# Performance work log

Hardware: AMD Instinct MI355X
Metric: run time of the kernel (lower is better)

The kernel has to match this reference:

```python
import jax, jax.numpy as jnp
import numpy as np

B, N, DIM, H, DH = 4, 16384, 256, 8, 32
INNER = H * DH
SCALE = DH ** -0.5


def setup_inputs() -> dict:
    key = jax.random.key(0)
    ks = jax.random.split(key, 15)
    g = lambda k, shape, s=0.02: jax.random.normal(k, shape, dtype=jnp.float32) * s
    return {
        "states": jax.random.normal(ks[0], (B, N, DIM), dtype=jnp.float32),
        "agent_qs": jax.random.normal(ks[1], (B, N, DIM), dtype=jnp.float32),
        "obs": jax.random.normal(ks[2], (B, N, DIM), dtype=jnp.float32),
        "Wq": g(ks[3], (DIM, INNER)), "bq": g(ks[4], (INNER,)),
        "Wk": g(ks[5], (DIM, INNER)), "bk": g(ks[6], (INNER,)),
        "Wv": g(ks[7], (DIM, INNER)), "bv": g(ks[8], (INNER,)),
        "wq_attn": g(ks[9], (DH,), 0.1),
        "wk_attn": g(ks[10], (DH,), 0.1),
        "Wr": g(ks[11], (DH, DH)), "br": g(ks[12], (DH,)),
        "Wout": g(ks[13], (INNER, DIM)), "bout": g(ks[14], (DIM,)),
    }


def _heads(t):
    # [b, n, h*d] -> [b, h, n, d]
    b, n, _ = t.shape
    return t.reshape(b, n, H, DH).transpose(0, 2, 1, 3)


def reference(states, agent_qs, obs, Wq, bq, Wk, bk, Wv, bv,
              wq_attn, wk_attn, Wr, br, Wout, bout):
    q = _heads(jnp.abs(states @ Wq + bq))   # b h n d
    k = _heads(agent_qs @ Wk + bk)          # b h n d
    v = _heads(obs @ Wv + bv)               # b h n d

    # additive attention pooling for global query
    q_attn = jax.nn.softmax(jnp.einsum('bhnd,d->bhn', q, wq_attn) * SCALE, axis=-1)
    global_q = jnp.einsum('bhn,bhnd->bhd', q_attn, q)  # b h d

    # gate keys with global query, pool against ORIGINAL k (k_aggr)
    k_gated = k * global_q[:, :, None, :]
    k_attn = jax.nn.softmax(jnp.einsum('bhnd,d->bhn', k_gated, wk_attn) * SCALE, axis=-1)
    global_k = jnp.einsum('bhn,bhnd->bhd', k_attn, k)  # b h d

    u = v * global_k[:, :, None, :]
    r = u @ Wr + br + q                      # b h n d
    r = r.transpose(0, 2, 1, 3).reshape(r.shape[0], r.shape[2], INNER)  # b n (h d)
    return r @ Wout + bout
```

## Files before the change

### kernel.cpp

```cpp
#include <hip/hip_runtime.h>
#include <hip/hip_bf16.h>

#define B_   4
#define N_   16384
#define T_   65536
static constexpr float SCALE_F = 0.17677669529663687f;

typedef __attribute__((ext_vector_type(8))) short bf16x8;
typedef __attribute__((ext_vector_type(4))) float f32x4;

static __device__ __forceinline__ unsigned pk2bf(float lo, float hi) {
    __hip_bfloat162 t = __float22bfloat162_rn(make_float2(lo, hi));
    union { __hip_bfloat162 h; unsigned u; } c; c.h = t; return c.u;
}
static __device__ __forceinline__ unsigned short f2bf(float f) {
    unsigned u = __float_as_uint(f);
    u += 0x7fffu + ((u >> 16) & 1u);
    return (unsigned short)(u >> 16);
}
static __device__ __forceinline__ void gl_lds16(const void* g, void* l) {
    __builtin_amdgcn_global_load_lds(
        (const __attribute__((address_space(1))) unsigned int*)g,
        (__attribute__((address_space(3))) unsigned int*)l, 16, 0, 0);
}

__global__ __launch_bounds__(256) void prep_w(
    const float* __restrict__ Wq, const float* __restrict__ Wk,
    const float* __restrict__ Wv, unsigned short* __restrict__ Wt)
{
    const int m = blockIdx.x;
    const float* W = (m == 0) ? Wq : (m == 1) ? Wk : Wv;
    unsigned short* dst = Wt + (size_t)m * 65536 + (size_t)threadIdx.x * 256;
    #pragma unroll 4
    for (int kb = 0; kb < 32; ++kb) {
        float v[8];
        #pragma unroll
        for (int e = 0; e < 8; ++e) v[e] = W[(kb*8 + e)*256 + threadIdx.x];
        uint4 w;
        w.x = pk2bf(v[0], v[1]); w.y = pk2bf(v[2], v[3]);
        w.z = pk2bf(v[4], v[5]); w.w = pk2bf(v[6], v[7]);
        *reinterpret_cast<uint4*>(dst + kb*8) = w;
    }
}

__global__ __launch_bounds__(256) void proj_mfma(
    const float* __restrict__ states, const float* __restrict__ agent_qs,
    const float* __restrict__ obs, const unsigned short* __restrict__ Wt,
    const float* __restrict__ bq, const float* __restrict__ bk,
    const float* __restrict__ bv,
    unsigned short* __restrict__ q_bf, unsigned short* __restrict__ k_bf,
    unsigned short* __restrict__ v_bf)
{
    __shared__ __align__(16) float As[2][64*32];

    const int tid = threadIdx.x;
    const int z  = blockIdx.y;
    const int t0 = blockIdx.x * 64;

    const float* X = (z == 0) ? states : (z == 1) ? agent_qs : obs;
    const unsigned short* Bt = Wt + (size_t)z * 65536;
    const float* bias = (z == 0) ? bq : (z == 1) ? bk : bv;
    unsigned short* Y = (z == 0) ? q_bf : (z == 1) ? k_bf : v_bf;
    const bool doabs = (z == 0);

    const int wid = tid >> 6, lane = tid & 63;
    const int l15 = lane & 15, g = lane >> 4;
    const int wc = wid;

    int ntrue[4];
    #pragma unroll
    for (int ni = 0; ni < 4; ++ni) {
        int np = ni*16 + l15;
        int c = (np & 32) | ((np & 12) << 1) | ((np & 16) >> 2) | (np & 3);
        ntrue[ni] = wc*64 + c;
    }

    const int srow_lane = lane >> 3;
    const int schunk = (lane & 7) ^ (lane >> 3);
    auto stageA = [&](int buf, int k0) {
        #pragma unroll
        for (int i = 0; i < 2; ++i) {
            int r = (wid*2 + i)*8 + srow_lane;
            const float* src = X + (size_t)(t0 + r)*256 + k0 + schunk*4;
            gl_lds16(src, &As[buf][(wid*2 + i)*256]);
        }
    };
    auto loadB = [&](bf16x8* breg, int k0) {
        #pragma unroll
        for (int ni = 0; ni < 4; ++ni)
            breg[ni] = *reinterpret_cast<const bf16x8*>(
                Bt + (size_t)ntrue[ni]*256 + k0 + g*8);
    };
    auto readA = [&](int buf, bf16x8* areg) {
        #pragma unroll
        for (int mi = 0; mi < 4; ++mi) {
            int m = mi*16 + l15;
            int x = m & 7;
            f32x4 lo = *reinterpret_cast<const f32x4*>(&As[buf][m*32 + ((2*g)  ^x)*4]);
            f32x4 hi = *reinterpret_cast<const f32x4*>(&As[buf][m*32 + ((2*g+1)^x)*4]);
            union { unsigned u[4]; bf16x8 v; } cc;
            cc.u[0] = pk2bf(lo[0], lo[1]);
            cc.u[1] = pk2bf(lo[2], lo[3]);
            cc.u[2] = pk2bf(hi[0], hi[1]);
            cc.u[3] = pk2bf(hi[2], hi[3]);
            areg[mi] = cc.v;
        }
    };

    f32x4 acc[4][4];
    #pragma unroll
    for (int mi = 0; mi < 4; ++mi)
        #pragma unroll
        for (int ni = 0; ni < 4; ++ni) acc[mi][ni] = (f32x4){0.f,0.f,0.f,0.f};

    bf16x8 bcur[4], bnxt[4];
    stageA(0, 0);
    loadB(bcur, 0);
    __syncthreads();

    int cur = 0;
    for (int s = 0; s < 8; ++s) {
        if (s < 7) { stageA(cur ^ 1, (s+1)*32); loadB(bnxt, (s+1)*32); }
        bf16x8 a[4];
        readA(cur, a);
        #pragma unroll
        for (int mi = 0; mi < 4; ++mi)
            #pragma unroll
            for (int ni = 0; ni < 4; ++ni)
                acc[mi][ni] = __builtin_amdgcn_mfma_f32_16x16x32_bf16(
                    bcur[ni], a[mi], acc[mi][ni], 0, 0, 0);
        __syncthreads();
        #pragma unroll
        for (int ni = 0; ni < 4; ++ni) bcur[ni] = bnxt[ni];
        cur ^= 1;
    }

    #pragma unroll
    for (int mi = 0; mi < 4; ++mi) {
        int m = t0 + mi*16 + l15;
        #pragma unroll
        for (int s = 0; s < 2; ++s) {
            int colb = wc*64 + s*32 + g*8;
            float4 b0 = *reinterpret_cast<const float4*>(bias + colb);
            float4 b1 = *reinterpret_cast<const float4*>(bias + colb + 4);
            float y0 = acc[mi][2*s  ][0] + b0.x;
            float y1 = acc[mi][2*s  ][1] + b0.y;
            float y2 = acc[mi][2*s  ][2] + b0.z;
            float y3 = acc[mi][2*s  ][3] + b0.w;
            float y4 = acc[mi][2*s+1][0] + b1.x;
            float y5 = acc[mi][2*s+1][1] + b1.y;
            float y6 = acc[mi][2*s+1][2] + b1.z;
            float y7 = acc[mi][2*s+1][3] + b1.w;
            if (doabs) {
                y0 = fabsf(y0); y1 = fabsf(y1); y2 = fabsf(y2); y3 = fabsf(y3);
                y4 = fabsf(y4); y5 = fabsf(y5); y6 = fabsf(y6); y7 = fabsf(y7);
            }
            uint4 pk;
            pk.x = pk2bf(y0, y1); pk.y = pk2bf(y2, y3);
            pk.z = pk2bf(y4, y5); pk.w = pk2bf(y6, y7);
            *reinterpret_cast<uint4*>(Y + (size_t)m*256 + colb) = pk;
        }
    }
}

__global__ __launch_bounds__(512) void pool_partial(
    const unsigned short* __restrict__ data,
    const float* __restrict__ wqa, const float* __restrict__ wka,
    const float* __restrict__ gq_in, float* __restrict__ part, int mode)
{
    const int bh = blockIdx.x, ch = blockIdx.y;
    const int b = bh >> 3, h = bh & 7;
    const int tid = threadIdx.x;

    __shared__ float coef[32];
    __shared__ float s_red[8];
    __shared__ float a_red[8][32];

    if (tid < 32) {
        float cc = (mode == 0) ? wqa[tid] : gq_in[bh*32 + tid] * wka[tid];
        coef[tid] = cc * SCALE_F;
    }
    __syncthreads();
    float cf[32];
    #pragma unroll
    for (int d = 0; d < 32; ++d) cf[d] = coef[d];

    float s = 0.f;
    float acc[32];
    #pragma unroll
    for (int d = 0; d < 32; ++d) acc[d] = 0.f;

    const unsigned short* base = data + (size_t)b * N_ * 256 + h * 32;
    for (int n = ch*2048 + tid; n < (ch + 1)*2048; n += 512) {
        const uint4* p = reinterpret_cast<const uint4*>(base + (size_t)n * 256);
        float qv[32];
        #pragma unroll
        for (int gg = 0; gg < 4; ++gg) {
            uint4 r = p[gg];
            unsigned w0 = r.x, w1 = r.y, w2 = r.z, w3 = r.w;
            qv[gg*8+0] = __uint_as_float(w0 << 16);
            qv[gg*8+1] = __uint_as_float(w0 & 0xffff0000u);
            qv[gg*8+2] = __uint_as_float(w1 << 16);
            qv[gg*8+3] = __uint_as_float(w1 & 0xffff0000u);
            qv[gg*8+4] = __uint_as_float(w2 << 16);
            qv[gg*8+5] = __uint_as_float(w2 & 0xffff0000u);
            qv[gg*8+6] = __uint_as_float(w3 << 16);
            qv[gg*8+7] = __uint_as_float(w3 & 0xffff0000u);
        }
        float l = 0.f;
        #pragma unroll
        for (int d = 0; d < 32; ++d) l = fmaf(qv[d], cf[d], l);
        float e = expf(l);
        s += e;
        #pragma unroll
        for (int d = 0; d < 32; ++d) acc[d] = fmaf(e, qv[d], acc[d]);
    }

    #pragma unroll
    for (int off = 1; off < 64; off <<= 1) {
        s += __shfl_xor(s, off);
        #pragma unroll
        for (int d = 0; d < 32; ++d) acc[d] += __shfl_xor(acc[d], off);
    }
    const int wave = tid >> 6, lane = tid & 63;
    if (lane == 0) {
        s_red[wave] = s;
        #pragma unroll
        for (int d = 0; d < 32; ++d) a_red[wave][d] = acc[d];
    }
    __syncthreads();
    if (tid < 32) {
        float num = 0.f, den = 0.f;
        #pragma unroll
        for (int w2 = 0; w2 < 8; ++w2) { num += a_red[w2][tid]; den += s_red[w2]; }
        part[(size_t)(bh*8 + ch)*40 + tid] = num;
        if (tid == 0) part[(size_t)(bh*8 + ch)*40 + 32] = den;
    }
}

__global__ __launch_bounds__(64) void pool_final(
    const float* __restrict__ part, float* __restrict__ outv)
{
    const int bh = blockIdx.x, d = threadIdx.x;
    if (d >= 32) return;
    float num = 0.f, den = 0.f;
    #pragma unroll
    for (int c = 0; c < 8; ++c) {
        num += part[(size_t)(bh*8 + c)*40 + d];
        den += part[(size_t)(bh*8 + c)*40 + 32];
    }
    outv[bh*32 + d] = num / den;
}

__global__ __launch_bounds__(256) void build_s1(
    const float* __restrict__ Wr, const float* __restrict__ br,
    const float* __restrict__ Wout, const float* __restrict__ bout,
    float* __restrict__ S1t, float* __restrict__ cvec)
{
    const int i = blockIdx.x, j = threadIdx.x;
    if (i < 256) {
        const int h = i >> 5, dd = i & 31;
        float s = 0.f;
        #pragma unroll 8
        for (int dp = 0; dp < 32; ++dp)
            s = fmaf(Wr[dd*32 + dp], Wout[(h*32 + dp)*256 + j], s);
        S1t[(size_t)j*256 + i] = s;
    } else {
        float cj = bout[j];
        for (int r = 0; r < 256; ++r) cj = fmaf(br[r & 31], Wout[r*256 + j], cj);
        cvec[j] = cj;
    }
}

__global__ __launch_bounds__(256) void build_wcat_t(
    const float* __restrict__ gk, const float* __restrict__ S1t,
    const float* __restrict__ Wout, unsigned short* __restrict__ Wcat_t)
{
    const int b = blockIdx.x, n = blockIdx.y, k = threadIdx.x;
    unsigned short* dst = Wcat_t + (size_t)(b*256 + n) * 512;
    dst[k]       = f2bf(gk[b*256 + k] * S1t[(size_t)n*256 + k]);
    dst[k + 256] = f2bf(Wout[(size_t)k*256 + n]);
}

__global__ __launch_bounds__(256) void out_mfma(
    const unsigned short* __restrict__ v_bf, const unsigned short* __restrict__ q_bf,
    const unsigned short* __restrict__ Wcat_t, const float* __restrict__ cvec,
    float* __restrict__ out)
{
    __shared__ __align__(16) unsigned short As[2][64*32];

    const int tid = threadIdx.x;
    const int t0 = blockIdx.x * 64;
    const int b  = t0 >> 14;
    const unsigned short* Wb = Wcat_t + (size_t)b * 256 * 512;

    const int wid = tid >> 6, lane = tid & 63;
    const int l15 = lane & 15, g = lane >> 4, wc = wid;

    const int sr = wid*16 + (lane >> 2);
    const int stc = (lane & 3) ^ (sr & 3) ^ ((sr >> 2) & 3);
    auto stageA = [&](int buf, int k0) {
        const unsigned short* src = (k0 < 256) ? v_bf : q_bf;
        int ks = k0 & 255;
        gl_lds16(src + (size_t)(t0 + sr)*256 + ks + stc*8, &As[buf][wid*512]);
    };
    auto loadB = [&](bf16x8* breg, int k0) {
        #pragma unroll
        for (int ni = 0; ni < 4; ++ni) {
            int nt = wc*64 + ni*16 + l15;
            breg[ni] = *reinterpret_cast<const bf16x8*>(
                Wb + (size_t)nt*512 + k0 + g*8);
        }
    };
    auto readA = [&](int buf, bf16x8* areg) {
        #pragma unroll
        for (int mi = 0; mi < 4; ++mi) {
            int m = mi*16 + l15;
            int cc = g ^ (m & 3) ^ ((m >> 2) & 3);
            areg[mi] = *reinterpret_cast<const bf16x8*>(&As[buf][m*32 + cc*8]);
        }
    };

    f32x4 acc[4][4];
    #pragma unroll
    for (int mi = 0; mi < 4; ++mi)
        #pragma unroll
        for (int ni = 0; ni < 4; ++ni) acc[mi][ni] = (f32x4){0.f,0.f,0.f,0.f};

    bf16x8 bcur[4], bnxt[4];
    stageA(0, 0);
    loadB(bcur, 0);
    __syncthreads();

    int cur = 0;
    for (int s = 0; s < 16; ++s) {
        if (s < 15) { stageA(cur ^ 1, (s+1)*32); loadB(bnxt, (s+1)*32); }
        bf16x8 a[4];
        readA(cur, a);
        #pragma unroll
        for (int mi = 0; mi < 4; ++mi)
            #pragma unroll
            for (int ni = 0; ni < 4; ++ni)
                acc[mi][ni] = __builtin_amdgcn_mfma_f32_16x16x32_bf16(
                    bcur[ni], a[mi], acc[mi][ni], 0, 0, 0);
        __syncthreads();
        #pragma unroll
        for (int ni = 0; ni < 4; ++ni) bcur[ni] = bnxt[ni];
        cur ^= 1;
    }

    #pragma unroll
    for (int ni = 0; ni < 4; ++ni) {
        int colb = wc*64 + ni*16 + g*4;
        float4 cv = *reinterpret_cast<const float4*>(cvec + colb);
        #pragma unroll
        for (int mi = 0; mi < 4; ++mi) {
            int m = t0 + mi*16 + l15;
            float4 o;
            o.x = acc[mi][ni][0] + cv.x;
            o.y = acc[mi][ni][1] + cv.y;
            o.z = acc[mi][ni][2] + cv.z;
            o.w = acc[mi][ni][3] + cv.w;
            *reinterpret_cast<float4*>(out + (size_t)m*256 + colb) = o;
        }
    }
}

extern "C" void kernel_launch(void* const* d_in, const int* in_sizes, int n_in,
                              void* d_out, int out_size, void* d_ws, size_t ws_size,
                              hipStream_t stream)
{
    const float* states   = (const float*)d_in[0];
    const float* agent_qs = (const float*)d_in[1];
    const float* obs      = (const float*)d_in[2];
    const float* Wq   = (const float*)d_in[3];
    const float* bq   = (const float*)d_in[4];
    const float* Wk   = (const float*)d_in[5];
    const float* bk   = (const float*)d_in[6];
    const float* Wv   = (const float*)d_in[7];
    const float* bv   = (const float*)d_in[8];
    const float* wq_attn = (const float*)d_in[9];
    const float* wk_attn = (const float*)d_in[10];
    const float* Wr   = (const float*)d_in[11];
    const float* br   = (const float*)d_in[12];
    const float* Wout = (const float*)d_in[13];
    const float* bout = (const float*)d_in[14];
    float* out = (float*)d_out;

    char* w = (char*)d_ws;
    unsigned short* q_bf = (unsigned short*)w; w += (size_t)T_ * 256 * 2;
    unsigned short* k_bf = (unsigned short*)w; w += (size_t)T_ * 256 * 2;
    unsigned short* v_bf = (unsigned short*)w; w += (size_t)T_ * 256 * 2;
    unsigned short* Wt_bf   = (unsigned short*)w; w += (size_t)3 * 65536 * 2;
    unsigned short* Wcat_t  = (unsigned short*)w; w += (size_t)4 * 256 * 512 * 2;
    float* gq   = (float*)w; w += 1024 * sizeof(float);
    float* gk   = (float*)w; w += 1024 * sizeof(float);
    float* part = (float*)w; w += (size_t)256 * 40 * sizeof(float);
    float* S1t  = (float*)w; w += (size_t)256 * 256 * sizeof(float);
    float* cvec = (float*)w; w += 256 * sizeof(float);

    prep_w<<<dim3(3), 256, 0, stream>>>(Wq, Wk, Wv, Wt_bf);
    proj_mfma<<<dim3(1024, 3), 256, 0, stream>>>(
        states, agent_qs, obs, Wt_bf, bq, bk, bv, q_bf, k_bf, v_bf);
    pool_partial<<<dim3(32, 8), 512, 0, stream>>>(q_bf, wq_attn, wk_attn, gq, part, 0);
    pool_final<<<dim3(32), 64, 0, stream>>>(part, gq);
    pool_partial<<<dim3(32, 8), 512, 0, stream>>>(k_bf, wq_attn, wk_attn, gq, part, 1);
    pool_final<<<dim3(32), 64, 0, stream>>>(part, gk);
    build_s1<<<dim3(257), 256, 0, stream>>>(Wr, br, Wout, bout, S1t, cvec);
    build_wcat_t<<<dim3(4, 256), 256, 0, stream>>>(gk, S1t, Wout, Wcat_t);
    out_mfma<<<dim3(1024), 256, 0, stream>>>(v_bf, q_bf, Wcat_t, cvec, out);
}
```

Before: 219.0 us.

## Triple-buffer GEMM staging and fold small reduction kernels into neighbors

Both MFMA GEMM kernels move from double to triple-buffered LDS staging. They use explicit vmcnt waits and raw barriers, so async global-to-LDS loads run two steps ahead and the full __syncthreads drain is gone. The pool_final kernels are removed, with their reductions folded into the next pool_partial and build_wcat_t. build_s1 is merged into the weight-prep kernel, cutting the launch count from 9 to 6. The cost is extra LDS per block, hand-tuned wait counts that must exactly match the number of outstanding loads, and some redundant reduction work repeated per thread.

```diff
diff --git a/kernel.cpp b/kernel.cpp
--- a/kernel.cpp
+++ b/kernel.cpp
@@ -9,6 +9,9 @@
 typedef __attribute__((ext_vector_type(8))) short bf16x8;
 typedef __attribute__((ext_vector_type(4))) float f32x4;
 
+#define BAR() __builtin_amdgcn_s_barrier()
+#define WAIT(vm) asm volatile("s_waitcnt vmcnt(" #vm ") lgkmcnt(0)" ::: "memory")
+
 static __device__ __forceinline__ unsigned pk2bf(float lo, float hi) {
     __hip_bfloat162 t = __float22bfloat162_rn(make_float2(lo, hi));
     union { __hip_bfloat162 h; unsigned u; } c; c.h = t; return c.u;
@@ -24,22 +27,41 @@
         (__attribute__((address_space(3))) unsigned int*)l, 16, 0, 0);
 }
 
-__global__ __launch_bounds__(256) void prep_w(
+__global__ __launch_bounds__(256) void prep_all(
     const float* __restrict__ Wq, const float* __restrict__ Wk,
-    const float* __restrict__ Wv, unsigned short* __restrict__ Wt)
-{
-    const int m = blockIdx.x;
-    const float* W = (m == 0) ? Wq : (m == 1) ? Wk : Wv;
-    unsigned short* dst = Wt + (size_t)m * 65536 + (size_t)threadIdx.x * 256;
-    #pragma unroll 4
-    for (int kb = 0; kb < 32; ++kb) {
-        float v[8];
-        #pragma unroll
-        for (int e = 0; e < 8; ++e) v[e] = W[(kb*8 + e)*256 + threadIdx.x];
-        uint4 w;
-        w.x = pk2bf(v[0], v[1]); w.y = pk2bf(v[2], v[3]);
-        w.z = pk2bf(v[4], v[5]); w.w = pk2bf(v[6], v[7]);
-        *reinterpret_cast<uint4*>(dst + kb*8) = w;
+    const float* __restrict__ Wv, unsigned short* __restrict__ Wt,
+    const float* __restrict__ Wr, const float* __restrict__ br,
+    const float* __restrict__ Wout, const float* __restrict__ bout,
+    float* __restrict__ S1t, float* __restrict__ cvec)
+{
+    const int blk = blockIdx.x;
+    if (blk < 3) {
+        const float* W = (blk == 0) ? Wq : (blk == 1) ? Wk : Wv;
+        unsigned short* dst = Wt + (size_t)blk * 65536 + (size_t)threadIdx.x * 256;
+        #pragma unroll 4
+        for (int kb = 0; kb < 32; ++kb) {
+            float v[8];
+            #pragma unroll
+            for (int e = 0; e < 8; ++e) v[e] = W[(kb*8 + e)*256 + threadIdx.x];
+            uint4 w;
+            w.x = pk2bf(v[0], v[1]); w.y = pk2bf(v[2], v[3]);
+            w.z = pk2bf(v[4], v[5]); w.w = pk2bf(v[6], v[7]);
+            *reinterpret_cast<uint4*>(dst + kb*8) = w;
+        }
+        return;
+    }
+    const int i = blk - 3, j = threadIdx.x;
+    if (i < 256) {
+        const int h = i >> 5, dd = i & 31;
+        float s = 0.f;
+        #pragma unroll 8
+        for (int dp = 0; dp < 32; ++dp)
+            s = fmaf(Wr[dd*32 + dp], Wout[(h*32 + dp)*256 + j], s);
+        S1t[(size_t)j*256 + i] = s;
+    } else {
+        float cj = bout[j];
+        for (int r = 0; r < 256; ++r) cj = fmaf(br[r & 31], Wout[r*256 + j], cj);
+        cvec[j] = cj;
     }
 }
 
@@ -51,7 +73,7 @@
     unsigned short* __restrict__ q_bf, unsigned short* __restrict__ k_bf,
     unsigned short* __restrict__ v_bf)
 {
-    __shared__ __align__(16) float As[2][64*32];
+    __shared__ __align__(16) float As[3][64*32];
 
     const int tid = threadIdx.x;
     const int z  = blockIdx.y;
@@ -77,72 +99,100 @@
 
     const int srow_lane = lane >> 3;
     const int schunk = (lane & 7) ^ (lane >> 3);
-    auto stageA = [&](int buf, int k0) {
+    auto stageA = [&](int buf, int step) {
+        const int k0 = step * 32;
         #pragma unroll
         for (int i = 0; i < 2; ++i) {
             int r = (wid*2 + i)*8 + srow_lane;
-            const float* src = X + (size_t)(t0 + r)*256 + k0 + schunk*4;
-            gl_lds16(src, &As[buf][(wid*2 + i)*256]);
-        }
-    };
-    auto loadB = [&](bf16x8* breg, int k0) {
+            gl_lds16(X + (size_t)(t0 + r)*256 + k0 + schunk*4,
+                     &As[buf][(wid*2 + i)*256]);
+        }
+    };
+    auto loadB = [&](bf16x8* breg, int step) {
+        const int k0 = step * 32;
         #pragma unroll
         for (int ni = 0; ni < 4; ++ni)
             breg[ni] = *reinterpret_cast<const bf16x8*>(
                 Bt + (size_t)ntrue[ni]*256 + k0 + g*8);
     };
-    auto readA = [&](int buf, bf16x8* areg) {
+    auto dsreadA = [&](int buf, f32x4* lo, f32x4* hi) {
         #pragma unroll
         for (int mi = 0; mi < 4; ++mi) {
             int m = mi*16 + l15;
             int x = m & 7;
-            f32x4 lo = *reinterpret_cast<const f32x4*>(&As[buf][m*32 + ((2*g)  ^x)*4]);
-            f32x4 hi = *reinterpret_cast<const f32x4*>(&As[buf][m*32 + ((2*g+1)^x)*4]);
+            lo[mi] = *reinterpret_cast<const f32x4*>(&As[buf][m*32 + ((2*g)  ^x)*4]);
+            hi[mi] = *reinterpret_cast<const f32x4*>(&As[buf][m*32 + ((2*g+1)^x)*4]);
+        }
+    };
+
+    f32x4 acc[4][4];
+    #pragma unroll
+    for (int mi = 0; mi < 4; ++mi)
+        #pragma unroll
+        for (int ni = 0; ni < 4; ++ni) acc[mi][ni] = (f32x4){0.f,0.f,0.f,0.f};
+
+    auto mfma_step = [&](const bf16x8* bb, const f32x4* lo, const f32x4* hi) {
+        bf16x8 a[4];
+        #pragma unroll
+        for (int mi = 0; mi < 4; ++mi) {
             union { unsigned u[4]; bf16x8 v; } cc;
-            cc.u[0] = pk2bf(lo[0], lo[1]);
-            cc.u[1] = pk2bf(lo[2], lo[3]);
-            cc.u[2] = pk2bf(hi[0], hi[1]);
-            cc.u[3] = pk2bf(hi[2], hi[3]);
-            areg[mi] = cc.v;
-        }
-    };
-
-    f32x4 acc[4][4];
-    #pragma unroll
-    for (int mi = 0; mi < 4; ++mi)
-        #pragma unroll
-        for (int ni = 0; ni < 4; ++ni) acc[mi][ni] = (f32x4){0.f,0.f,0.f,0.f};
-
-    bf16x8 bcur[4], bnxt[4];
-    stageA(0, 0);
-    loadB(bcur, 0);
-    __syncthreads();
-
-    int cur = 0;
-    for (int s = 0; s < 8; ++s) {
-        if (s < 7) { stageA(cur ^ 1, (s+1)*32); loadB(bnxt, (s+1)*32); }
-        bf16x8 a[4];
-        readA(cur, a);
+            cc.u[0] = pk2bf(lo[mi][0], lo[mi][1]);
+            cc.u[1] = pk2bf(lo[mi][2], lo[mi][3]);
+            cc.u[2] = pk2bf(hi[mi][0], hi[mi][1]);
+            cc.u[3] = pk2bf(hi[mi][2], hi[mi][3]);
+            a[mi] = cc.v;
+        }
         #pragma unroll
         for (int mi = 0; mi < 4; ++mi)
             #pragma unroll
             for (int ni = 0; ni < 4; ++ni)
                 acc[mi][ni] = __builtin_amdgcn_mfma_f32_16x16x32_bf16(
-                    bcur[ni], a[mi], acc[mi][ni], 0, 0, 0);
-        __syncthreads();
-        #pragma unroll
-        for (int ni = 0; ni < 4; ++ni) bcur[ni] = bnxt[ni];
-        cur ^= 1;
-    }
-
-    #pragma unroll
-    for (int mi = 0; mi < 4; ++mi) {
-        int m = t0 + mi*16 + l15;
-        #pragma unroll
-        for (int s = 0; s < 2; ++s) {
-            int colb = wc*64 + s*32 + g*8;
-            float4 b0 = *reinterpret_cast<const float4*>(bias + colb);
-            float4 b1 = *reinterpret_cast<const float4*>(bias + colb + 4);
+                    bb[ni], a[mi], acc[mi][ni], 0, 0, 0);
+    };
+
+    bf16x8 bcur[4], bn[4];
+    loadB(bcur, 0);
+    stageA(0, 0);
+    stageA(1, 1);
+    WAIT(0); BAR();
+
+    int br_ = 0, bw_ = 2;
+    for (int s = 0; s < 6; ++s) {
+        loadB(bn, s + 1);
+        f32x4 lo[4], hi[4];
+        dsreadA(br_, lo, hi);
+        stageA(bw_, s + 2);
+        mfma_step(bcur, lo, hi);
+        WAIT(6); BAR();
+        #pragma unroll
+        for (int ni = 0; ni < 4; ++ni) bcur[ni] = bn[ni];
+        br_ = (br_ == 2) ? 0 : br_ + 1;
+        bw_ = (bw_ == 2) ? 0 : bw_ + 1;
+    }
+    {
+        loadB(bn, 7);
+        f32x4 lo[4], hi[4];
+        dsreadA(br_, lo, hi);
+        mfma_step(bcur, lo, hi);
+        WAIT(4); BAR();
+        #pragma unroll
+        for (int ni = 0; ni < 4; ++ni) bcur[ni] = bn[ni];
+        br_ = (br_ == 2) ? 0 : br_ + 1;
+    }
+    {
+        f32x4 lo[4], hi[4];
+        dsreadA(br_, lo, hi);
+        mfma_step(bcur, lo, hi);
+    }
+
+    #pragma unroll
+    for (int s = 0; s < 2; ++s) {
+        int colb = wc*64 + s*32 + g*8;
+        float4 b0 = *reinterpret_cast<const float4*>(bias + colb);
+        float4 b1 = *reinterpret_cast<const float4*>(bias + colb + 4);
+        #pragma unroll
+        for (int mi = 0; mi < 4; ++mi) {
+            int m = t0 + mi*16 + l15;
             float y0 = acc[mi][2*s  ][0] + b0.x;
             float y1 = acc[mi][2*s  ][1] + b0.y;
             float y2 = acc[mi][2*s  ][2] + b0.z;
@@ -166,7 +216,7 @@
 __global__ __launch_bounds__(512) void pool_partial(
     const unsigned short* __restrict__ data,
     const float* __restrict__ wqa, const float* __restrict__ wka,
-    const float* __restrict__ gq_in, float* __restrict__ part, int mode)
+    const float* __restrict__ part_in, float* __restrict__ part_out, int mode)
 {
     const int bh = blockIdx.x, ch = blockIdx.y;
     const int b = bh >> 3, h = bh & 7;
@@ -177,7 +227,17 @@
     __shared__ float a_red[8][32];
 
     if (tid < 32) {
-        float cc = (mode == 0) ? wqa[tid] : gq_in[bh*32 + tid] * wka[tid];
+        float cc;
+        if (mode == 0) cc = wqa[tid];
+        else {
+            float num = 0.f, den = 0.f;
+            #pragma unroll
+            for (int c = 0; c < 8; ++c) {
+                num += part_in[(size_t)(bh*8 + c)*40 + tid];
+                den += part_in[(size_t)(bh*8 + c)*40 + 32];
+            }
+            cc = (num / den) * wka[tid];
+        }
         coef[tid] = cc * SCALE_F;
     }
     __syncthreads();
@@ -233,52 +293,26 @@
         float num = 0.f, den = 0.f;
         #pragma unroll
         for (int w2 = 0; w2 < 8; ++w2) { num += a_red[w2][tid]; den += s_red[w2]; }
-        part[(size_t)(bh*8 + ch)*40 + tid] = num;
-        if (tid == 0) part[(size_t)(bh*8 + ch)*40 + 32] = den;
-    }
-}
-
-__global__ __launch_bounds__(64) void pool_final(
-    const float* __restrict__ part, float* __restrict__ outv)
-{
-    const int bh = blockIdx.x, d = threadIdx.x;
-    if (d >= 32) return;
+        part_out[(size_t)(bh*8 + ch)*40 + tid] = num;
+        if (tid == 0) part_out[(size_t)(bh*8 + ch)*40 + 32] = den;
+    }
+}
+
+__global__ __launch_bounds__(256) void build_wcat_t(
+    const float* __restrict__ part_k, const float* __restrict__ S1t,
+    const float* __restrict__ Wout, unsigned short* __restrict__ Wcat_t)
+{
+    const int b = blockIdx.x, n = blockIdx.y, k = threadIdx.x;
+    const int h = k >> 5, d = k & 31;
     float num = 0.f, den = 0.f;
     #pragma unroll
     for (int c = 0; c < 8; ++c) {
-        num += part[(size_t)(bh*8 + c)*40 + d];
-        den += part[(size_t)(bh*8 + c)*40 + 32];
-    }
-    outv[bh*32 + d] = num / den;
-}
-
-__global__ __launch_bounds__(256) void build_s1(
-    const float* __restrict__ Wr, const float* __restrict__ br,
-    const float* __restrict__ Wout, const float* __restrict__ bout,
-    float* __restrict__ S1t, float* __restrict__ cvec)
-{
-    const int i = blockIdx.x, j = threadIdx.x;
-    if (i < 256) {
-        const int h = i >> 5, dd = i & 31;
-        float s = 0.f;
-        #pragma unroll 8
-        for (int dp = 0; dp < 32; ++dp)
-            s = fmaf(Wr[dd*32 + dp], Wout[(h*32 + dp)*256 + j], s);
-        S1t[(size_t)j*256 + i] = s;
-    } else {
-        float cj = bout[j];
-        for (int r = 0; r < 256; ++r) cj = fmaf(br[r & 31], Wout[r*256 + j], cj);
-        cvec[j] = cj;
-    }
-}
-
-__global__ __launch_bounds__(256) void build_wcat_t(
-    const float* __restrict__ gk, const float* __restrict__ S1t,
-    const float* __restrict__ Wout, unsigned short* __restrict__ Wcat_t)
-{
-    const int b = blockIdx.x, n = blockIdx.y, k = threadIdx.x;
+        num += part_k[(size_t)((b*8 + h)*8 + c)*40 + d];
+        den += part_k[(size_t)((b*8 + h)*8 + c)*40 + 32];
+    }
+    const float gkv = num / den;
     unsigned short* dst = Wcat_t + (size_t)(b*256 + n) * 512;
-    dst[k]       = f2bf(gk[b*256 + k] * S1t[(size_t)n*256 + k]);
+    dst[k]       = f2bf(gkv * S1t[(size_t)n*256 + k]);
     dst[k + 256] = f2bf(Wout[(size_t)k*256 + n]);
 }
 
@@ -287,7 +321,7 @@
     const unsigned short* __restrict__ Wcat_t, const float* __restrict__ cvec,
     float* __restrict__ out)
 {
-    __shared__ __align__(16) unsigned short As[2][64*32];
+    __shared__ __align__(16) unsigned short As[3][64*32];
 
     const int tid = threadIdx.x;
     const int t0 = blockIdx.x * 64;
@@ -299,12 +333,14 @@
 
     const int sr = wid*16 + (lane >> 2);
     const int stc = (lane & 3) ^ (sr & 3) ^ ((sr >> 2) & 3);
-    auto stageA = [&](int buf, int k0) {
+    auto stageA = [&](int buf, int step) {
+        const int k0 = step * 32;
         const unsigned short* src = (k0 < 256) ? v_bf : q_bf;
         int ks = k0 & 255;
         gl_lds16(src + (size_t)(t0 + sr)*256 + ks + stc*8, &As[buf][wid*512]);
     };
-    auto loadB = [&](bf16x8* breg, int k0) {
+    auto loadB = [&](bf16x8* breg, int step) {
+        const int k0 = step * 32;
         #pragma unroll
         for (int ni = 0; ni < 4; ++ni) {
             int nt = wc*64 + ni*16 + l15;
@@ -312,42 +348,55 @@
                 Wb + (size_t)nt*512 + k0 + g*8);
         }
     };
-    auto readA = [&](int buf, bf16x8* areg) {
+
+    f32x4 acc[4][4];
+    #pragma unroll
+    for (int mi = 0; mi < 4; ++mi)
+        #pragma unroll
+        for (int ni = 0; ni < 4; ++ni) acc[mi][ni] = (f32x4){0.f,0.f,0.f,0.f};
+
+    auto step_body = [&](int buf, const bf16x8* bb) {
+        bf16x8 a[4];
         #pragma unroll
         for (int mi = 0; mi < 4; ++mi) {
             int m = mi*16 + l15;
             int cc = g ^ (m & 3) ^ ((m >> 2) & 3);
-            areg[mi] = *reinterpret_cast<const bf16x8*>(&As[buf][m*32 + cc*8]);
-        }
-    };
-
-    f32x4 acc[4][4];
-    #pragma unroll
-    for (int mi = 0; mi < 4; ++mi)
-        #pragma unroll
-        for (int ni = 0; ni < 4; ++ni) acc[mi][ni] = (f32x4){0.f,0.f,0.f,0.f};
-
-    bf16x8 bcur[4], bnxt[4];
-    stageA(0, 0);
-    loadB(bcur, 0);
-    __syncthreads();
-
-    int cur = 0;
-    for (int s = 0; s < 16; ++s) {
-        if (s < 15) { stageA(cur ^ 1, (s+1)*32); loadB(bnxt, (s+1)*32); }
-        bf16x8 a[4];
-        readA(cur, a);
+            a[mi] = *reinterpret_cast<const bf16x8*>(&As[buf][m*32 + cc*8]);
+        }
         #pragma unroll
         for (int mi = 0; mi < 4; ++mi)
             #pragma unroll
             for (int ni = 0; ni < 4; ++ni)
                 acc[mi][ni] = __builtin_amdgcn_mfma_f32_16x16x32_bf16(
-                    bcur[ni], a[mi], acc[mi][ni], 0, 0, 0);
-        __syncthreads();
-        #pragma unroll
-        for (int ni = 0; ni < 4; ++ni) bcur[ni] = bnxt[ni];
-        cur ^= 1;
-    }
+                    bb[ni], a[mi], acc[mi][ni], 0, 0, 0);
+    };
+
+    bf16x8 bcur[4], bn[4];
+    loadB(bcur, 0);
+    stageA(0, 0);
+    stageA(1, 1);
+    WAIT(0); BAR();
+
+    int br_ = 0, bw_ = 2;
+    for (int s = 0; s < 14; ++s) {
+        loadB(bn, s + 1);
+        stageA(bw_, s + 2);
+        step_body(br_, bcur);
+        WAIT(5); BAR();
+        #pragma unroll
+        for (int ni = 0; ni < 4; ++ni) bcur[ni] = bn[ni];
+        br_ = (br_ == 2) ? 0 : br_ + 1;
+        bw_ = (bw_ == 2) ? 0 : bw_ + 1;
+    }
+    {
+        loadB(bn, 15);
+        step_body(br_, bcur);
+        WAIT(4); BAR();
+        #pragma unroll
+        for (int ni = 0; ni < 4; ++ni) bcur[ni] = bn[ni];
+        br_ = (br_ == 2) ? 0 : br_ + 1;
+    }
+    step_body(br_, bcur);
 
     #pragma unroll
     for (int ni = 0; ni < 4; ++ni) {
@@ -393,20 +442,19 @@
     unsigned short* v_bf = (unsigned short*)w; w += (size_t)T_ * 256 * 2;
     unsigned short* Wt_bf   = (unsigned short*)w; w += (size_t)3 * 65536 * 2;
     unsigned short* Wcat_t  = (unsigned short*)w; w += (size_t)4 * 256 * 512 * 2;
-    float* gq   = (float*)w; w += 1024 * sizeof(float);
-    float* gk   = (float*)w; w += 1024 * sizeof(float);
-    float* part = (float*)w; w += (size_t)256 * 40 * sizeof(float);
+    float* part_q = (float*)w; w += (size_t)256 * 40 * sizeof(float);
+    float* part_k = (float*)w; w += (size_t)256 * 40 * sizeof(float);
     float* S1t  = (float*)w; w += (size_t)256 * 256 * sizeof(float);
     float* cvec = (float*)w; w += 256 * sizeof(float);
 
-    prep_w<<<dim3(3), 256, 0, stream>>>(Wq, Wk, Wv, Wt_bf);
+    prep_all<<<dim3(260), 256, 0, stream>>>(Wq, Wk, Wv, Wt_bf,
+                                            Wr, br, Wout, bout, S1t, cvec);
     proj_mfma<<<dim3(1024, 3), 256, 0, stream>>>(
         states, agent_qs, obs, Wt_bf, bq, bk, bv, q_bf, k_bf, v_bf);
-    pool_partial<<<dim3(32, 8), 512, 0, stream>>>(q_bf, wq_attn, wk_attn, gq, part, 0);
-    pool_final<<<dim3(32), 64, 0, stream>>>(part, gq);
-    pool_partial<<<dim3(32, 8), 512, 0, stream>>>(k_bf, wq_attn, wk_attn, gq, part, 1);
-    pool_final<<<dim3(32), 64, 0, stream>>>(part, gk);
-    build_s1<<<dim3(257), 256, 0, stream>>>(Wr, br, Wout, bout, S1t, cvec);
-    build_wcat_t<<<dim3(4, 256), 256, 0, stream>>>(gk, S1t, Wout, Wcat_t);
+    pool_partial<<<dim3(32, 8), 512, 0, stream>>>(q_bf, wq_attn, wk_attn,
+                                                  part_q, part_q, 0);
+    pool_partial<<<dim3(32, 8), 512, 0, stream>>>(k_bf, wq_attn, wk_attn,
+                                                  part_q, part_k, 1);
+    build_wcat_t<<<dim3(4, 256), 256, 0, stream>>>(part_k, S1t, Wout, Wcat_t);
     out_mfma<<<dim3(1024), 256, 0, stream>>>(v_bf, q_bf, Wcat_t, cvec, out);
 }
```

After: 206.1 us. 1.06x faster.
